# Optimization experiments

Hardware: AMD Instinct MI355X
Metric: run time of the kernel (lower is better)

## Reference

```python
import jax, jax.numpy as jnp
import numpy as np

B, S, H, NH = 2, 2048, 1024, 16
HD = H // NH
ROTARY_DIM = 64
EPS = 1e-5
MINUS_INF = -10000.0


def _apply_rotary(q, k, rotary_dim):
    # q, k: [B, S, NH, HD]; GPT-NeoX style rotate_half on first rotary_dim dims
    pos = jnp.arange(S, dtype=jnp.float32)
    inv_freq = 1.0 / (10000.0 ** (jnp.arange(0, rotary_dim, 2, dtype=jnp.float32) / rotary_dim))
    freqs = pos[:, None] * inv_freq[None, :]                      # [S, rd/2]
    cos = jnp.concatenate([jnp.cos(freqs)] * 2, -1)[None, :, None, :]  # [1,S,1,rd]
    sin = jnp.concatenate([jnp.sin(freqs)] * 2, -1)[None, :, None, :]

    def rot(t):
        t_rot, t_pass = t[..., :rotary_dim], t[..., rotary_dim:]
        t1, t2 = jnp.split(t_rot, 2, axis=-1)
        rotated = jnp.concatenate([-t2, t1], axis=-1)
        return jnp.concatenate([t_rot * cos + rotated * sin, t_pass], axis=-1)

    return rot(q), rot(k)


def setup_inputs() -> dict:
    key = jax.random.key(0)
    ks = jax.random.split(key, 6)
    w_scale = 0.02
    return {
        "x": jax.random.normal(ks[0], (B, S, H), jnp.float32),
        "input_mask": jnp.ones((B, S), jnp.int32),
        "norm_w": jnp.ones((H,), jnp.float32),
        "norm_b": jnp.zeros((H,), jnp.float32),
        "attn_qkvw": jax.random.normal(ks[1], (H, 3 * H), jnp.float32) * w_scale,
        "attn_qkvb": jax.random.normal(ks[2], (3 * H,), jnp.float32) * w_scale,
        "attn_ow": jax.random.normal(ks[3], (H, H), jnp.float32) * w_scale,
        "attn_ob": jax.random.normal(ks[4], (H,), jnp.float32) * w_scale,
    }


def reference(x, input_mask, norm_w, norm_b, attn_qkvw, attn_qkvb, attn_ow, attn_ob):
    # pre-layernorm (qkv_gemm path with config.pre_layer_norm)
    mu = x.mean(-1, keepdims=True)
    var = x.var(-1, keepdims=True)
    xn = (x - mu) * jax.lax.rsqrt(var + EPS) * norm_w + norm_b

    # fused QKV projection
    qkv = xn @ attn_qkvw + attn_qkvb                       # [B,S,3H]
    q, k, v = jnp.split(qkv, 3, axis=-1)
    q = q.reshape(B, S, NH, HD)
    k = k.reshape(B, S, NH, HD)
    v = v.reshape(B, S, NH, HD)

    # rotary embedding on q,k
    q, k = _apply_rotary(q, k, ROTARY_DIM)

    # scaled scores + mask bias (1 - mask) * -10000 + triangular masking
    scale = 1.0 / np.sqrt(HD).astype(np.float32)
    scores = jnp.einsum("bqhd,bkhd->bhqk", q, k) * scale   # [B,NH,S,S]
    mask_bias = (1.0 - input_mask.astype(scores.dtype)) * MINUS_INF
    scores = scores + mask_bias[:, None, None, :]
    causal = jnp.tril(jnp.ones((S, S), bool))
    scores = jnp.where(causal[None, None], scores, MINUS_INF)

    probs = jax.nn.softmax(scores, axis=-1)
    ctx = jnp.einsum("bhqk,bkhd->bqhd", probs, v).reshape(B, S, H)

    # output projection (vector_matmul + bias)
    return ctx @ attn_ow + attn_ob
```

## Files before the change

### kernel.cpp

```cpp
#include <hip/hip_runtime.h>
#include <hip/hip_bf16.h>

#define B_  2
#define S_  2048
#define H_  1024
#define NH_ 16
#define HD_ 64
#define T_  (B_*S_)
#define H3_ (3*H_)

typedef float  floatx4 __attribute__((ext_vector_type(4)));
typedef __bf16 bf16x8  __attribute__((ext_vector_type(8)));

__device__ inline unsigned short f2bf_rn(float f) {
    union { float f; unsigned int u; } v; v.f = f;
    unsigned int u = v.u;
    u += 0x7fffu + ((u >> 16) & 1u);
    return (unsigned short)(u >> 16);
}
__device__ inline unsigned short f2bf_tr(float f) {
    union { float f; unsigned int u; } v; v.f = f;
    return (unsigned short)(v.u >> 16);
}
__device__ inline floatx4 fzero4() { floatx4 v; v[0]=0.f; v[1]=0.f; v[2]=0.f; v[3]=0.f; return v; }

__device__ inline void gload_lds16(const unsigned short* g, unsigned short* l) {
    __builtin_amdgcn_global_load_lds((const __attribute__((address_space(1))) unsigned int*)g,
                                     (__attribute__((address_space(3))) unsigned int*)l,
                                     16, 0, 0);
}

#define TLD 72
__global__ __launch_bounds__(256) void cvt_both_k(const float* __restrict__ qkvw,
                                                  const float* __restrict__ ow,
                                                  unsigned short* __restrict__ qkvwT,
                                                  unsigned short* __restrict__ owT) {
    __shared__ unsigned short Ts[64 * TLD];
    int id = blockIdx.x;
    const float* W; unsigned short* Wt; int N, nb, kb;
    if (id < 768) { W = qkvw; Wt = qkvwT; N = H3_; nb = (id % 48) * 64; kb = (id / 48) * 64; }
    else { id -= 768; W = ow; Wt = owT; N = H_; nb = (id % 16) * 64; kb = (id / 16) * 64; }
    const int K = H_;
    const int tid = threadIdx.x;
    #pragma unroll
    for (int p = 0; p < 4; p++) {
        const int krow = kb + p * 16 + (tid >> 4);
        const int ncol = (tid & 15) * 4;
        const float4 w = *reinterpret_cast<const float4*>(&W[(size_t)krow * N + nb + ncol]);
        Ts[(ncol + 0) * TLD + p * 16 + (tid >> 4)] = f2bf_rn(w.x);
        Ts[(ncol + 1) * TLD + p * 16 + (tid >> 4)] = f2bf_rn(w.y);
        Ts[(ncol + 2) * TLD + p * 16 + (tid >> 4)] = f2bf_rn(w.z);
        Ts[(ncol + 3) * TLD + p * 16 + (tid >> 4)] = f2bf_rn(w.w);
    }
    __syncthreads();
    #pragma unroll
    for (int p = 0; p < 2; p++) {
        const int n = (tid >> 3) + p * 32;
        const int k8 = (tid & 7) * 8;
        const uint4 v = *reinterpret_cast<const uint4*>(&Ts[n * TLD + k8]);
        *reinterpret_cast<uint4*>(&Wt[(size_t)(nb + n) * K + kb + k8]) = v;
    }
}

__global__ __launch_bounds__(256) void layernorm_k(const float* __restrict__ x,
                                                   const float* __restrict__ w,
                                                   const float* __restrict__ b,
                                                   unsigned short* __restrict__ xn) {
    const int t   = blockIdx.x;
    const int tid = threadIdx.x;
    const float4 v = reinterpret_cast<const float4*>(x + (size_t)t * H_)[tid];
    float s  = v.x + v.y + v.z + v.w;
    float s2 = v.x*v.x + v.y*v.y + v.z*v.z + v.w*v.w;
    for (int off = 32; off > 0; off >>= 1) {
        s  += __shfl_down(s,  off, 64);
        s2 += __shfl_down(s2, off, 64);
    }
    __shared__ float red[8];
    const int wave = tid >> 6, lane = tid & 63;
    if (lane == 0) { red[wave] = s; red[4 + wave] = s2; }
    __syncthreads();
    if (tid == 0) {
        red[0] = red[0] + red[1] + red[2] + red[3];
        red[4] = red[4] + red[5] + red[6] + red[7];
    }
    __syncthreads();
    const float mean = red[0] * (1.f / H_);
    const float var  = red[4] * (1.f / H_) - mean * mean;
    const float rstd = rsqrtf(var + 1e-5f);
    const float4 wv = reinterpret_cast<const float4*>(w)[tid];
    const float4 bv = reinterpret_cast<const float4*>(b)[tid];
    ushort4 o = make_ushort4(f2bf_rn((v.x - mean) * rstd * wv.x + bv.x),
                             f2bf_rn((v.y - mean) * rstd * wv.y + bv.y),
                             f2bf_rn((v.z - mean) * rstd * wv.z + bv.z),
                             f2bf_rn((v.w - mean) * rstd * wv.w + bv.w));
    reinterpret_cast<ushort4*>(xn + (size_t)t * H_)[tid] = o;
}

#define BM 128
#define BN 128

__device__ inline void gemm_core(const unsigned short* __restrict__ A,
                                 const unsigned short* __restrict__ Bt,
                                 int K, int mBase, int nBase,
                                 int tid, floatx4 acc[4][4],
                                 unsigned short* As0, unsigned short* As1,
                                 unsigned short* Bs0, unsigned short* Bs1) {
    const int lane = tid & 63;
    const int wave = tid >> 6;
    const int wr = wave >> 1, wc = wave & 1;
    const int srow = lane >> 2;
    const int scol = (lane & 3) * 8;
    const int mrow = lane & 15;
    const int koff = (lane >> 4) * 8;

    for (int kb = 0; kb < K; kb += 64) {
        __syncthreads();
        #pragma unroll
        for (int p = 0; p < 2; p++) {
            const int r = wave * 16 + p * 64;
            const size_t ga = (size_t)(mBase + r + srow) * K + kb + scol;
            const size_t gb = (size_t)(nBase + r + srow) * K + kb + scol;
            gload_lds16(&A [ga],      &As0[r * 32]);
            gload_lds16(&A [ga + 32], &As1[r * 32]);
            gload_lds16(&Bt[gb],      &Bs0[r * 32]);
            gload_lds16(&Bt[gb + 32], &Bs1[r * 32]);
        }
        __syncthreads();

        #pragma unroll
        for (int half = 0; half < 2; half++) {
            const unsigned short* As = half ? As1 : As0;
            const unsigned short* Bs = half ? Bs1 : Bs0;
            bf16x8 afrag[4], bfrag[4];
            #pragma unroll
            for (int mt = 0; mt < 4; mt++)
                afrag[mt] = *reinterpret_cast<const bf16x8*>(&As[(wr * 64 + mt * 16 + mrow) * 32 + koff]);
            #pragma unroll
            for (int nt = 0; nt < 4; nt++)
                bfrag[nt] = *reinterpret_cast<const bf16x8*>(&Bs[(wc * 64 + nt * 16 + mrow) * 32 + koff]);
            #pragma unroll
            for (int mt = 0; mt < 4; mt++)
                #pragma unroll
                for (int nt = 0; nt < 4; nt++)
                    acc[mt][nt] = __builtin_amdgcn_mfma_f32_16x16x32_bf16(afrag[mt], bfrag[nt], acc[mt][nt], 0, 0, 0);
        }
    }
}

__global__ __launch_bounds__(256) void gemm_qkv_k(const unsigned short* __restrict__ A,
                                                  const unsigned short* __restrict__ Bt,
                                                  const float* __restrict__ bias,
                                                  unsigned short* __restrict__ Qo,
                                                  unsigned short* __restrict__ Ko,
                                                  unsigned short* __restrict__ Vto) {
    __shared__ unsigned short As0[BM * 32], As1[BM * 32];
    __shared__ unsigned short Bs0[BN * 32], Bs1[BN * 32];

    const int tid  = threadIdx.x;
    const int lane = tid & 63;
    const int wave = tid >> 6;
    const int wr = wave >> 1, wc = wave & 1;
    const int mBase = blockIdx.y * BM;
    const int nBase = blockIdx.x * BN;

    floatx4 acc[4][4];
    #pragma unroll
    for (int i = 0; i < 4; i++)
        #pragma unroll
        for (int j = 0; j < 4; j++) acc[i][j] = fzero4();

    gemm_core(A, Bt, H_, mBase, nBase, tid, acc, As0, As1, Bs0, Bs1);

    const int col0 = lane & 15;
    const int r0   = (lane >> 4) * 4;
    const int hg   = (nBase + wc * 64) >> 6;
    const int sec  = hg >> 4;
    const int h    = hg & 15;

    float bs[4];
    #pragma unroll
    for (int nt = 0; nt < 4; nt++) bs[nt] = bias[nBase + wc * 64 + nt * 16 + col0];

    if (sec < 2) {
        unsigned short* dst = (sec == 0) ? Qo : Ko;
        const float if0 = __expf((float)col0        * (-0.2878231366f));
        const float if1 = __expf((float)(16 + col0) * (-0.2878231366f));
        #pragma unroll
        for (int mt = 0; mt < 4; mt++) {
            #pragma unroll
            for (int reg = 0; reg < 4; reg++) {
                const int t  = mBase + wr * 64 + mt * 16 + r0 + reg;
                const int bb = t >> 11;
                const int s  = t & (S_ - 1);
                float sn0, cs0, sn1, cs1;
                __sincosf((float)s * if0, &sn0, &cs0);
                __sincosf((float)s * if1, &sn1, &cs1);
                const float v0 = acc[mt][0][reg] + bs[0];
                const float v1 = acc[mt][1][reg] + bs[1];
                const float v2 = acc[mt][2][reg] + bs[2];
                const float v3 = acc[mt][3][reg] + bs[3];
                const float o0 = v0 * cs0 - v2 * sn0;
                const float o1 = v1 * cs1 - v3 * sn1;
                const float o2 = v2 * cs0 + v0 * sn0;
                const float o3 = v3 * cs1 + v1 * sn1;
                const size_t rb = ((size_t)(bb * NH_ + h) * S_ + s) * HD_;
                dst[rb +      col0] = f2bf_rn(o0);
                dst[rb + 16 + col0] = f2bf_rn(o1);
                dst[rb + 32 + col0] = f2bf_rn(o2);
                dst[rb + 48 + col0] = f2bf_rn(o3);
            }
        }
    } else {
        #pragma unroll
        for (int mt = 0; mt < 4; mt++) {
            const int t0 = mBase + wr * 64 + mt * 16 + r0;
            const int bb = t0 >> 11;
            const int s0 = t0 & (S_ - 1);
            #pragma unroll
            for (int nt = 0; nt < 4; nt++) {
                const int d = nt * 16 + col0;
                ushort4 o;
                o.x = f2bf_rn(acc[mt][nt][0] + bs[nt]);
                o.y = f2bf_rn(acc[mt][nt][1] + bs[nt]);
                o.z = f2bf_rn(acc[mt][nt][2] + bs[nt]);
                o.w = f2bf_rn(acc[mt][nt][3] + bs[nt]);
                *reinterpret_cast<ushort4*>(&Vto[((size_t)(bb * NH_ + h) * HD_ + d) * S_ + s0]) = o;
            }
        }
    }
}

__global__ __launch_bounds__(256) void gemm_proj_k(const unsigned short* __restrict__ A,
                                                   const unsigned short* __restrict__ Bt,
                                                   const float* __restrict__ bias,
                                                   float* __restrict__ Cf,
                                                   int M, int N, int K) {
    __shared__ unsigned short As0[BM * 32], As1[BM * 32];
    __shared__ unsigned short Bs0[BN * 32], Bs1[BN * 32];

    const int tid  = threadIdx.x;
    const int lane = tid & 63;
    const int wave = tid >> 6;
    const int wr = wave >> 1, wc = wave & 1;
    const int mBase = blockIdx.y * BM;
    const int nBase = blockIdx.x * BN;

    floatx4 acc[4][4];
    #pragma unroll
    for (int i = 0; i < 4; i++)
        #pragma unroll
        for (int j = 0; j < 4; j++) acc[i][j] = fzero4();

    gemm_core(A, Bt, K, mBase, nBase, tid, acc, As0, As1, Bs0, Bs1);

    const int col0 = lane & 15;
    const int r0   = (lane >> 4) * 4;
    #pragma unroll
    for (int mt = 0; mt < 4; mt++) {
        #pragma unroll
        for (int nt = 0; nt < 4; nt++) {
            const int gcol = nBase + wc * 64 + nt * 16 + col0;
            const float bsv = bias[gcol];
            #pragma unroll
            for (int reg = 0; reg < 4; reg++) {
                const int grow = mBase + wr * 64 + mt * 16 + r0 + reg;
                Cf[(size_t)grow * N + gcol] = acc[mt][nt][reg] + bsv;
            }
        }
    }
}

#define ALD 72
#define SCL2 0.1803368801f
#define MNEG -14427.0f

__global__ __launch_bounds__(256, 3) void attn_k(const unsigned short* __restrict__ Q,
                                                 const unsigned short* __restrict__ Kg,
                                                 const unsigned short* __restrict__ Vt,
                                                 const int* __restrict__ mask,
                                                 unsigned short* __restrict__ ctx) {
    const int id = blockIdx.x;
    const int bh = id & 31;
    const int v  = 31 - (id >> 5);
    const int b  = bh >> 4;
    const int h  = bh & 15;
    const int tid  = threadIdx.x;
    const int lane = tid & 63;
    const int wave = tid >> 6;

    __shared__ unsigned short Ks [2][64 * ALD];
    __shared__ unsigned short Vts[2][64 * ALD];
    __shared__ unsigned short Ps[4][16 * ALD];

    const size_t base = (size_t)bh * S_ * HD_;
    const int qbase = v * 64 + wave * 16;
    const int mrow = lane & 15;
    const int koff = (lane >> 4) * 8;
    const int r0   = (lane >> 4) * 4;
    const int col0 = lane & 15;

    bf16x8 qf0 = *reinterpret_cast<const bf16x8*>(&Q[base + (size_t)(qbase + mrow) * HD_ + koff]);
    bf16x8 qf1 = *reinterpret_cast<const bf16x8*>(&Q[base + (size_t)(qbase + mrow) * HD_ + 32 + koff]);

    bf16x8 onesf;
    {
        const __bf16 ov = (__bf16)((mrow == 0) ? 1.f : 0.f);
        #pragma unroll
        for (int q = 0; q < 8; q++) onesf[q] = ov;
    }

    floatx4 Oacc[4];
    floatx4 Lacc = fzero4();
    #pragma unroll
    for (int nt = 0; nt < 4; nt++) Oacc[nt] = fzero4();

    const int srow = tid >> 3;
    const int scol = (tid & 7) * 8;

    uint4 k00, k01, k10, k11, v00, v01, v10, v11;
    float mb00, mb01, mb02, mb03, mb10, mb11, mb12, mb13;
#define PF_TILE(TT, KR0, KR1, VR0, VR1, M0, M1, M2, M3) do {                                   \
        const int kb_ = (TT) * 64;                                                             \
        KR0 = *reinterpret_cast<const uint4*>(&Kg[base + (size_t)(kb_ + srow)      * HD_ + scol]); \
        KR1 = *reinterpret_cast<const uint4*>(&Kg[base + (size_t)(kb_ + srow + 32) * HD_ + scol]); \
        VR0 = *reinterpret_cast<const uint4*>(&Vt[base + (size_t)srow        * S_ + kb_ + scol]);  \
        VR1 = *reinterpret_cast<const uint4*>(&Vt[base + (size_t)(srow + 32) * S_ + kb_ + scol]);  \
        M0 = (1.f - (float)mask[b * S_ + kb_ +  0 + col0]) * MNEG;                             \
        M1 = (1.f - (float)mask[b * S_ + kb_ + 16 + col0]) * MNEG;                             \
        M2 = (1.f - (float)mask[b * S_ + kb_ + 32 + col0]) * MNEG;                             \
        M3 = (1.f - (float)mask[b * S_ + kb_ + 48 + col0]) * MNEG;                             \
    } while (0)
#define PREFETCH_MACRO(MI) do {                                                                \
        const int t0_ = min(2 * (MI), v);                                                      \
        const int t1_ = min(2 * (MI) + 1, v);                                                  \
        PF_TILE(t0_, k00, k01, v00, v01, mb00, mb01, mb02, mb03);                              \
        PF_TILE(t1_, k10, k11, v10, v11, mb10, mb11, mb12, mb13);                              \
    } while (0)

    const int nmac = (v + 2) >> 1;
    PREFETCH_MACRO(0);

    unsigned short* pw = Ps[wave];

    for (int mi = 0; mi < nmac; mi++) {
        if (mi) __syncthreads();
        *reinterpret_cast<uint4*>(&Ks [0][ srow       * ALD + scol]) = k00;
        *reinterpret_cast<uint4*>(&Ks [0][(srow + 32) * ALD + scol]) = k01;
        *reinterpret_cast<uint4*>(&Ks [1][ srow       * ALD + scol]) = k10;
        *reinterpret_cast<uint4*>(&Ks [1][(srow + 32) * ALD + scol]) = k11;
        *reinterpret_cast<uint4*>(&Vts[0][ srow       * ALD + scol]) = v00;
        *reinterpret_cast<uint4*>(&Vts[0][(srow + 32) * ALD + scol]) = v01;
        *reinterpret_cast<uint4*>(&Vts[1][ srow       * ALD + scol]) = v10;
        *reinterpret_cast<uint4*>(&Vts[1][(srow + 32) * ALD + scol]) = v11;
        __syncthreads();
        const float mc00 = mb00, mc01 = mb01, mc02 = mb02, mc03 = mb03;
        const float mc10 = mb10, mc11 = mb11, mc12 = mb12, mc13 = mb13;
        if (mi + 1 < nmac) PREFETCH_MACRO(mi + 1);

        #pragma unroll
        for (int half = 0; half < 2; half++) {
            const int kt = 2 * mi + half;
            if (half && kt > v) continue;
            const int kb = kt * 64;
            const unsigned short* ks = Ks [half];
            const unsigned short* vs = Vts[half];
            const float c0 = half ? mc10 : mc00;
            const float c1 = half ? mc11 : mc01;
            const float c2 = half ? mc12 : mc02;
            const float c3 = half ? mc13 : mc03;

            floatx4 sc[4];
            #pragma unroll
            for (int nt = 0; nt < 4; nt++) {
                const bf16x8 kf0 = *reinterpret_cast<const bf16x8*>(&ks[(nt * 16 + mrow) * ALD + koff]);
                const bf16x8 kf1 = *reinterpret_cast<const bf16x8*>(&ks[(nt * 16 + mrow) * ALD + 32 + koff]);
                floatx4 c = fzero4();
                c = __builtin_amdgcn_mfma_f32_16x16x32_bf16(qf0, kf0, c, 0, 0, 0);
                c = __builtin_amdgcn_mfma_f32_16x16x32_bf16(qf1, kf1, c, 0, 0, 0);
                sc[nt] = c;
            }
            #pragma unroll
            for (int nt = 0; nt < 4; nt++) {
                const float mbv = (nt == 0) ? c0 : (nt == 1) ? c1 : (nt == 2) ? c2 : c3;
                #pragma unroll
                for (int reg = 0; reg < 4; reg++)
                    sc[nt][reg] = sc[nt][reg] * SCL2 + mbv;
            }
            if (kt == v) {
                #pragma unroll
                for (int nt = 0; nt < 4; nt++) {
                    const int key = kb + nt * 16 + col0;
                    #pragma unroll
                    for (int reg = 0; reg < 4; reg++)
                        if (key > qbase + r0 + reg) sc[nt][reg] = MNEG;
                }
            }
            #pragma unroll
            for (int nt = 0; nt < 4; nt++)
                #pragma unroll
                for (int reg = 0; reg < 4; reg++)
                    pw[(r0 + reg) * ALD + nt * 16 + col0] = f2bf_tr(exp2f(sc[nt][reg]));
            const bf16x8 p0 = *reinterpret_cast<const bf16x8*>(&pw[mrow * ALD + koff]);
            const bf16x8 p1 = *reinterpret_cast<const bf16x8*>(&pw[mrow * ALD + 32 + koff]);
            #pragma unroll
            for (int nt = 0; nt < 4; nt++) {
                const bf16x8 vf0 = *reinterpret_cast<const bf16x8*>(&vs[(nt * 16 + mrow) * ALD + koff]);
                const bf16x8 vf1 = *reinterpret_cast<const bf16x8*>(&vs[(nt * 16 + mrow) * ALD + 32 + koff]);
                Oacc[nt] = __builtin_amdgcn_mfma_f32_16x16x32_bf16(p0, vf0, Oacc[nt], 0, 0, 0);
                Oacc[nt] = __builtin_amdgcn_mfma_f32_16x16x32_bf16(p1, vf1, Oacc[nt], 0, 0, 0);
            }
            Lacc = __builtin_amdgcn_mfma_f32_16x16x32_bf16(p0, onesf, Lacc, 0, 0, 0);
            Lacc = __builtin_amdgcn_mfma_f32_16x16x32_bf16(p1, onesf, Lacc, 0, 0, 0);
        }
    }
#undef PREFETCH_MACRO
#undef PF_TILE

    float rl[4];
    #pragma unroll
    for (int reg = 0; reg < 4; reg++) {
        const float lsum = __shfl(Lacc[reg], lane & 48, 64);
        rl[reg] = 1.f / lsum;
    }
    #pragma unroll
    for (int nt = 0; nt < 4; nt++)
        #pragma unroll
        for (int reg = 0; reg < 4; reg++) {
            const int q = qbase + r0 + reg;
            const int d = nt * 16 + col0;
            ctx[((size_t)b * S_ + q) * H_ + h * HD_ + d] = f2bf_rn(Oacc[nt][reg] * rl[reg]);
        }
}

extern "C" void kernel_launch(void* const* d_in, const int* in_sizes, int n_in,
                              void* d_out, int out_size, void* d_ws, size_t ws_size,
                              hipStream_t stream) {
    const float* x     = (const float*)d_in[0];
    const int*   mask  = (const int*)d_in[1];
    const float* normw = (const float*)d_in[2];
    const float* normb = (const float*)d_in[3];
    const float* qkvw  = (const float*)d_in[4];
    const float* qkvb  = (const float*)d_in[5];
    const float* ow    = (const float*)d_in[6];
    const float* ob    = (const float*)d_in[7];
    float* out = (float*)d_out;

    char* ws = (char*)d_ws;
    unsigned short* xn_bf   = (unsigned short*)(ws);
    unsigned short* qkvwT   = (unsigned short*)(ws + (8ull  << 20));
    unsigned short* owT     = (unsigned short*)(ws + (14ull << 20));
    unsigned short* Qb      = (unsigned short*)(ws + (16ull << 20));
    unsigned short* Kb      = (unsigned short*)(ws + (24ull << 20));
    unsigned short* Vtb     = (unsigned short*)(ws + (32ull << 20));
    unsigned short* ctx_bf  = (unsigned short*)(ws + (40ull << 20));

    cvt_both_k<<<1024, 256, 0, stream>>>(qkvw, ow, qkvwT, owT);
    layernorm_k<<<T_, 256, 0, stream>>>(x, normw, normb, xn_bf);
    gemm_qkv_k<<<dim3(H3_ / BN, T_ / BM), 256, 0, stream>>>(xn_bf, qkvwT, qkvb, Qb, Kb, Vtb);
    attn_k<<<1024, 256, 0, stream>>>(Qb, Kb, Vtb, mask, ctx_bf);
    gemm_proj_k<<<dim3(H_ / BN, T_ / BM), 256, 0, stream>>>(ctx_bf, owT, ob, out, T_, H_, H_);
}
```

Before: 200.6 us.

## Compute transposed scores in attention to keep P in registers, drop LDS round-trip

```diff
diff --git a/kernel.cpp b/kernel.cpp
--- a/kernel.cpp
+++ b/kernel.cpp
@@ -18,11 +18,18 @@
     u += 0x7fffu + ((u >> 16) & 1u);
     return (unsigned short)(u >> 16);
 }
-__device__ inline unsigned short f2bf_tr(float f) {
-    union { float f; unsigned int u; } v; v.f = f;
-    return (unsigned short)(v.u >> 16);
-}
 __device__ inline floatx4 fzero4() { floatx4 v; v[0]=0.f; v[1]=0.f; v[2]=0.f; v[3]=0.f; return v; }
+
+__device__ inline unsigned int cvtpk_bf16(float lo, float hi) {
+    unsigned int r;
+    asm("v_cvt_pk_bf16_f32 %0, %1, %2" : "=v"(r) : "v"(lo), "v"(hi));
+    return r;
+}
+__device__ inline float bfsum2(unsigned int u) {
+    union { unsigned int i; float f; } a, c;
+    a.i = u << 16; c.i = u & 0xffff0000u;
+    return a.f + c.f;
+}
 
 __device__ inline void gload_lds16(const unsigned short* g, unsigned short* l) {
     __builtin_amdgcn_global_load_lds((const __attribute__((address_space(1))) unsigned int*)g,
@@ -274,7 +281,7 @@
 #define SCL2 0.1803368801f
 #define MNEG -14427.0f
 
-__global__ __launch_bounds__(256, 3) void attn_k(const unsigned short* __restrict__ Q,
+__global__ __launch_bounds__(256, 4) void attn_k(const unsigned short* __restrict__ Q,
                                                  const unsigned short* __restrict__ Kg,
                                                  const unsigned short* __restrict__ Vt,
                                                  const int* __restrict__ mask,
@@ -290,57 +297,43 @@
 
     __shared__ unsigned short Ks [2][64 * ALD];
     __shared__ unsigned short Vts[2][64 * ALD];
-    __shared__ unsigned short Ps[4][16 * ALD];
 
     const size_t base = (size_t)bh * S_ * HD_;
     const int qbase = v * 64 + wave * 16;
-    const int mrow = lane & 15;
+    const int r16  = lane & 15;
     const int koff = (lane >> 4) * 8;
-    const int r0   = (lane >> 4) * 4;
-    const int col0 = lane & 15;
-
-    bf16x8 qf0 = *reinterpret_cast<const bf16x8*>(&Q[base + (size_t)(qbase + mrow) * HD_ + koff]);
-    bf16x8 qf1 = *reinterpret_cast<const bf16x8*>(&Q[base + (size_t)(qbase + mrow) * HD_ + 32 + koff]);
-
-    bf16x8 onesf;
-    {
-        const __bf16 ov = (__bf16)((mrow == 0) ? 1.f : 0.f);
-        #pragma unroll
-        for (int q = 0; q < 8; q++) onesf[q] = ov;
-    }
-
-    floatx4 Oacc[4];
-    floatx4 Lacc = fzero4();
-    #pragma unroll
-    for (int nt = 0; nt < 4; nt++) Oacc[nt] = fzero4();
+    const int g8   = (lane >> 4) * 8;
+    const int qcol = qbase + r16;
+
+    const bf16x8 qf0 = *reinterpret_cast<const bf16x8*>(&Q[base + (size_t)(qbase + r16) * HD_ + koff]);
+    const bf16x8 qf1 = *reinterpret_cast<const bf16x8*>(&Q[base + (size_t)(qbase + r16) * HD_ + 32 + koff]);
+
+    floatx4 Ot[4];
+    #pragma unroll
+    for (int db = 0; db < 4; db++) Ot[db] = fzero4();
+    float Lp = 0.f;
 
     const int srow = tid >> 3;
     const int scol = (tid & 7) * 8;
+    const int pi = ((srow & 12) << 1) | (srow & 3) | (((srow >> 4) & 1) << 2);
 
     uint4 k00, k01, k10, k11, v00, v01, v10, v11;
-    float mb00, mb01, mb02, mb03, mb10, mb11, mb12, mb13;
-#define PF_TILE(TT, KR0, KR1, VR0, VR1, M0, M1, M2, M3) do {                                   \
+#define PF_TILE(TT, KR0, KR1, VR0, VR1) do {                                                   \
         const int kb_ = (TT) * 64;                                                             \
-        KR0 = *reinterpret_cast<const uint4*>(&Kg[base + (size_t)(kb_ + srow)      * HD_ + scol]); \
-        KR1 = *reinterpret_cast<const uint4*>(&Kg[base + (size_t)(kb_ + srow + 32) * HD_ + scol]); \
+        KR0 = *reinterpret_cast<const uint4*>(&Kg[base + (size_t)(kb_ + pi)      * HD_ + scol]); \
+        KR1 = *reinterpret_cast<const uint4*>(&Kg[base + (size_t)(kb_ + 32 + pi) * HD_ + scol]); \
         VR0 = *reinterpret_cast<const uint4*>(&Vt[base + (size_t)srow        * S_ + kb_ + scol]);  \
         VR1 = *reinterpret_cast<const uint4*>(&Vt[base + (size_t)(srow + 32) * S_ + kb_ + scol]);  \
-        M0 = (1.f - (float)mask[b * S_ + kb_ +  0 + col0]) * MNEG;                             \
-        M1 = (1.f - (float)mask[b * S_ + kb_ + 16 + col0]) * MNEG;                             \
-        M2 = (1.f - (float)mask[b * S_ + kb_ + 32 + col0]) * MNEG;                             \
-        M3 = (1.f - (float)mask[b * S_ + kb_ + 48 + col0]) * MNEG;                             \
     } while (0)
 #define PREFETCH_MACRO(MI) do {                                                                \
         const int t0_ = min(2 * (MI), v);                                                      \
         const int t1_ = min(2 * (MI) + 1, v);                                                  \
-        PF_TILE(t0_, k00, k01, v00, v01, mb00, mb01, mb02, mb03);                              \
-        PF_TILE(t1_, k10, k11, v10, v11, mb10, mb11, mb12, mb13);                              \
+        PF_TILE(t0_, k00, k01, v00, v01);                                                      \
+        PF_TILE(t1_, k10, k11, v10, v11);                                                      \
     } while (0)
 
     const int nmac = (v + 2) >> 1;
     PREFETCH_MACRO(0);
-
-    unsigned short* pw = Ps[wave];
 
     for (int mi = 0; mi < nmac; mi++) {
         if (mi) __syncthreads();
@@ -353,8 +346,6 @@
         *reinterpret_cast<uint4*>(&Vts[1][ srow       * ALD + scol]) = v10;
         *reinterpret_cast<uint4*>(&Vts[1][(srow + 32) * ALD + scol]) = v11;
         __syncthreads();
-        const float mc00 = mb00, mc01 = mb01, mc02 = mb02, mc03 = mb03;
-        const float mc10 = mb10, mc11 = mb11, mc12 = mb12, mc13 = mb13;
         if (mi + 1 < nmac) PREFETCH_MACRO(mi + 1);
 
         #pragma unroll
@@ -364,72 +355,67 @@
             const int kb = kt * 64;
             const unsigned short* ks = Ks [half];
             const unsigned short* vs = Vts[half];
-            const float c0 = half ? mc10 : mc00;
-            const float c1 = half ? mc11 : mc01;
-            const float c2 = half ? mc12 : mc02;
-            const float c3 = half ? mc13 : mc03;
-
-            floatx4 sc[4];
-            #pragma unroll
-            for (int nt = 0; nt < 4; nt++) {
-                const bf16x8 kf0 = *reinterpret_cast<const bf16x8*>(&ks[(nt * 16 + mrow) * ALD + koff]);
-                const bf16x8 kf1 = *reinterpret_cast<const bf16x8*>(&ks[(nt * 16 + mrow) * ALD + 32 + koff]);
-                floatx4 c = fzero4();
-                c = __builtin_amdgcn_mfma_f32_16x16x32_bf16(qf0, kf0, c, 0, 0, 0);
-                c = __builtin_amdgcn_mfma_f32_16x16x32_bf16(qf1, kf1, c, 0, 0, 0);
-                sc[nt] = c;
-            }
-            #pragma unroll
-            for (int nt = 0; nt < 4; nt++) {
-                const float mbv = (nt == 0) ? c0 : (nt == 1) ? c1 : (nt == 2) ? c2 : c3;
+
+            #pragma unroll
+            for (int w = 0; w < 2; w++) {
+                float p[2][4];
                 #pragma unroll
-                for (int reg = 0; reg < 4; reg++)
-                    sc[nt][reg] = sc[nt][reg] * SCL2 + mbv;
-            }
-            if (kt == v) {
+                for (int ab = 0; ab < 2; ab++) {
+                    const int nt = w * 2 + ab;
+                    const bf16x8 kf0 = *reinterpret_cast<const bf16x8*>(&ks[(nt * 16 + r16) * ALD + koff]);
+                    const bf16x8 kf1 = *reinterpret_cast<const bf16x8*>(&ks[(nt * 16 + r16) * ALD + 32 + koff]);
+                    floatx4 c = fzero4();
+                    c = __builtin_amdgcn_mfma_f32_16x16x32_bf16(kf0, qf0, c, 0, 0, 0);
+                    c = __builtin_amdgcn_mfma_f32_16x16x32_bf16(kf1, qf1, c, 0, 0, 0);
+                    const int kbase = kb + w * 32 + ab * 4 + g8;
+                    const int4 mm = *reinterpret_cast<const int4*>(&mask[b * S_ + kbase]);
+                    float sc0 = c[0] * SCL2 + (1.f - (float)mm.x) * MNEG;
+                    float sc1 = c[1] * SCL2 + (1.f - (float)mm.y) * MNEG;
+                    float sc2 = c[2] * SCL2 + (1.f - (float)mm.z) * MNEG;
+                    float sc3 = c[3] * SCL2 + (1.f - (float)mm.w) * MNEG;
+                    if (kt == v) {
+                        if (kbase + 0 > qcol) sc0 = MNEG;
+                        if (kbase + 1 > qcol) sc1 = MNEG;
+                        if (kbase + 2 > qcol) sc2 = MNEG;
+                        if (kbase + 3 > qcol) sc3 = MNEG;
+                    }
+                    p[ab][0] = exp2f(sc0);
+                    p[ab][1] = exp2f(sc1);
+                    p[ab][2] = exp2f(sc2);
+                    p[ab][3] = exp2f(sc3);
+                }
+                const unsigned int u0 = cvtpk_bf16(p[0][0], p[0][1]);
+                const unsigned int u1 = cvtpk_bf16(p[0][2], p[0][3]);
+                const unsigned int u2 = cvtpk_bf16(p[1][0], p[1][1]);
+                const unsigned int u3 = cvtpk_bf16(p[1][2], p[1][3]);
+                Lp += (bfsum2(u0) + bfsum2(u1)) + (bfsum2(u2) + bfsum2(u3));
+                union { uint4 u; bf16x8 v; } pf;
+                pf.u.x = u0; pf.u.y = u1; pf.u.z = u2; pf.u.w = u3;
                 #pragma unroll
-                for (int nt = 0; nt < 4; nt++) {
-                    const int key = kb + nt * 16 + col0;
-                    #pragma unroll
-                    for (int reg = 0; reg < 4; reg++)
-                        if (key > qbase + r0 + reg) sc[nt][reg] = MNEG;
+                for (int db = 0; db < 4; db++) {
+                    const bf16x8 vf = *reinterpret_cast<const bf16x8*>(&vs[(db * 16 + r16) * ALD + w * 32 + koff]);
+                    Ot[db] = __builtin_amdgcn_mfma_f32_16x16x32_bf16(vf, pf.v, Ot[db], 0, 0, 0);
                 }
             }
-            #pragma unroll
-            for (int nt = 0; nt < 4; nt++)
-                #pragma unroll
-                for (int reg = 0; reg < 4; reg++)
-                    pw[(r0 + reg) * ALD + nt * 16 + col0] = f2bf_tr(exp2f(sc[nt][reg]));
-            const bf16x8 p0 = *reinterpret_cast<const bf16x8*>(&pw[mrow * ALD + koff]);
-            const bf16x8 p1 = *reinterpret_cast<const bf16x8*>(&pw[mrow * ALD + 32 + koff]);
-            #pragma unroll
-            for (int nt = 0; nt < 4; nt++) {
-                const bf16x8 vf0 = *reinterpret_cast<const bf16x8*>(&vs[(nt * 16 + mrow) * ALD + koff]);
-                const bf16x8 vf1 = *reinterpret_cast<const bf16x8*>(&vs[(nt * 16 + mrow) * ALD + 32 + koff]);
-                Oacc[nt] = __builtin_amdgcn_mfma_f32_16x16x32_bf16(p0, vf0, Oacc[nt], 0, 0, 0);
-                Oacc[nt] = __builtin_amdgcn_mfma_f32_16x16x32_bf16(p1, vf1, Oacc[nt], 0, 0, 0);
-            }
-            Lacc = __builtin_amdgcn_mfma_f32_16x16x32_bf16(p0, onesf, Lacc, 0, 0, 0);
-            Lacc = __builtin_amdgcn_mfma_f32_16x16x32_bf16(p1, onesf, Lacc, 0, 0, 0);
         }
     }
 #undef PREFETCH_MACRO
 #undef PF_TILE
 
-    float rl[4];
-    #pragma unroll
-    for (int reg = 0; reg < 4; reg++) {
-        const float lsum = __shfl(Lacc[reg], lane & 48, 64);
-        rl[reg] = 1.f / lsum;
-    }
-    #pragma unroll
-    for (int nt = 0; nt < 4; nt++)
-        #pragma unroll
-        for (int reg = 0; reg < 4; reg++) {
-            const int q = qbase + r0 + reg;
-            const int d = nt * 16 + col0;
-            ctx[((size_t)b * S_ + q) * H_ + h * HD_ + d] = f2bf_rn(Oacc[nt][reg] * rl[reg]);
-        }
+    float lsum = Lp;
+    lsum += __shfl_xor(lsum, 16, 64);
+    lsum += __shfl_xor(lsum, 32, 64);
+    const float rl = 1.f / lsum;
+    const int r4 = (lane >> 4) * 4;
+    #pragma unroll
+    for (int db = 0; db < 4; db++) {
+        ushort4 o;
+        o.x = f2bf_rn(Ot[db][0] * rl);
+        o.y = f2bf_rn(Ot[db][1] * rl);
+        o.z = f2bf_rn(Ot[db][2] * rl);
+        o.w = f2bf_rn(Ot[db][3] * rl);
+        *reinterpret_cast<ushort4*>(&ctx[((size_t)b * S_ + qcol) * H_ + h * HD_ + db * 16 + r4]) = o;
+    }
 }
 
 extern "C" void kernel_launch(void* const* d_in, const int* in_sizes, int n_in,
```

After: 209.2 us. 4.3% more time.
